# Optimization experiments

Hardware: AMD Instinct MI355X
Metric: run time of the kernel (lower is better)

Reference implementation:

```python
import jax, jax.numpy as jnp
import numpy as np

D_MODEL = 256
NUM_HEADS = 8
D_HEAD = D_MODEL // NUM_HEADS  # 32


def setup_inputs() -> dict:
    key = jax.random.key(0)
    ks = jax.random.split(key, 7)
    N, WH = 8, 2048
    s = 1.0 / np.sqrt(D_MODEL)
    return {
        "x": jax.random.normal(ks[0], (N, WH, D_MODEL), dtype=jnp.float32),
        "Wq": jax.random.normal(ks[1], (D_MODEL, D_MODEL), dtype=jnp.float32) * s,
        "bq": jnp.zeros((D_MODEL,), dtype=jnp.float32),
        "Wk": jax.random.normal(ks[2], (D_MODEL, D_MODEL), dtype=jnp.float32) * s,
        "bk": jnp.zeros((D_MODEL,), dtype=jnp.float32),
        "Wv": jax.random.normal(ks[3], (D_MODEL, D_MODEL), dtype=jnp.float32) * s,
        "bv": jnp.zeros((D_MODEL,), dtype=jnp.float32),
    }


def _mhsa(x, Wq, bq, Wk, bk, Wv, bv):
    N, WH, C = x.shape
    # QKV projections; reshape to (N, heads, WH, d_head)
    def split_heads(t):
        return t.reshape(N, WH, NUM_HEADS, D_HEAD).transpose(0, 2, 1, 3)
    Q = split_heads(x @ Wq + bq)
    K = split_heads(x @ Wk + bk)
    V = split_heads(x @ Wv + bv)
    # FAITHFUL to source: logits /= d_k**(-0.5)  ==  logits * sqrt(d_k)
    logits = jnp.einsum("nhqd,nhkd->nhqk", Q, K) * jnp.sqrt(jnp.float32(D_HEAD))
    attn = jax.nn.softmax(logits, axis=-1)  # dropout p=0.1 is identity in eval
    x_attn = jnp.einsum("nhqk,nhkd->nhqd", attn, V)
    x_attn = x_attn.transpose(0, 2, 1, 3).reshape(N, WH, C)
    # drop_path is identity in eval mode; residual add
    return x_attn + x


def reference(x, Wq, bq, Wk, bk, Wv, bv):
    return _mhsa(x, Wq, bq, Wk, bk, Wv, bv)
```

## Files before the change

### kernel.cpp

```cpp
#include <hip/hip_runtime.h>
#include <math.h>

#define WH 2048
#define DM 256
#define NHD 8
#define DH 32
#define NB 8

typedef __attribute__((ext_vector_type(8))) short short8;
typedef __attribute__((ext_vector_type(4))) short short4v;
typedef __attribute__((ext_vector_type(4))) float f32x4;

__device__ __forceinline__ unsigned short bf16_rn(float f) {
    unsigned u = __float_as_uint(f);
    return (unsigned short)((u + 0x8000u) >> 16);
}
__device__ __forceinline__ float bf16_to_f(unsigned short h) {
    return __uint_as_float(((unsigned)h) << 16);
}
__device__ __forceinline__ unsigned pack_bf16_rn(float f1, float f0) {
    return __builtin_amdgcn_perm(__float_as_uint(f1) + 0x8000u,
                                 __float_as_uint(f0) + 0x8000u, 0x07060302);
}
__device__ __forceinline__ void glds16(const void* g, void* l) {
    __builtin_amdgcn_global_load_lds(
        (const __attribute__((address_space(1))) unsigned int*)g,
        (__attribute__((address_space(3))) unsigned int*)l, 16, 0, 0);
}

__global__ __launch_bounds__(256) void xprep(
    const float* __restrict__ X,
    unsigned short* __restrict__ Xhi, unsigned short* __restrict__ Xlo)
{
    const size_t i = ((size_t)blockIdx.x * 256 + threadIdx.x) * 8;
    float4 a = *(const float4*)&X[i];
    float4 b = *(const float4*)&X[i + 4];
    float v[8] = {a.x, a.y, a.z, a.w, b.x, b.y, b.z, b.w};
    short8 hi, lo;
    #pragma unroll
    for (int e = 0; e < 8; e++) {
        unsigned short hb = bf16_rn(v[e]);
        hi[e] = (short)hb;
        lo[e] = (short)bf16_rn(v[e] - bf16_to_f(hb));
    }
    *(short8*)&Xhi[i] = hi;
    *(short8*)&Xlo[i] = lo;
}

__global__ __launch_bounds__(256) void wprep(
    const float* __restrict__ Wq, const float* __restrict__ Wk,
    const float* __restrict__ Wv,
    unsigned short* __restrict__ WThi, unsigned short* __restrict__ WTlo)
{
    const int z = blockIdx.y;
    const float* W = (z == 0) ? Wq : ((z == 1) ? Wk : Wv);
    const size_t zoff = (size_t)z * DM * DM;
    const int tg = blockIdx.x * 256 + threadIdx.x;
    #pragma unroll
    for (int j = 0; j < 4; j++) {
        const int f = tg + j * 4096;
        const int k  = f >> 6;
        const int n0 = (f & 63) * 4;
        float4 v = *(const float4*)&W[(size_t)k * DM + n0];
        float vv[4] = {v.x, v.y, v.z, v.w};
        #pragma unroll
        for (int i = 0; i < 4; i++) {
            unsigned short hb = bf16_rn(vv[i]);
            WThi[zoff + (size_t)(n0 + i) * DM + k] = hb;
            WTlo[zoff + (size_t)(n0 + i) * DM + k] = bf16_rn(vv[i] - bf16_to_f(hb));
        }
    }
}

#define ASTR 40
__global__ __launch_bounds__(256) void qkv_mfma(
    const unsigned short* __restrict__ Xhi, const unsigned short* __restrict__ Xlo,
    const unsigned short* __restrict__ WThi, const unsigned short* __restrict__ WTlo,
    const float* __restrict__ bq, const float* __restrict__ bk, const float* __restrict__ bv,
    unsigned short* __restrict__ Qhi, unsigned short* __restrict__ Qlo,
    unsigned short* __restrict__ Khi, unsigned short* __restrict__ Klo,
    unsigned short* __restrict__ Vt)
{
    __shared__ __align__(16) char arena[40960];
    unsigned short* Ah = (unsigned short*)arena;
    unsigned short* Al = Ah + 128 * ASTR;
    unsigned short* Bh = Al + 128 * ASTR;
    unsigned short* Bl = Bh + 128 * ASTR;

    const int z = blockIdx.z;
    const float* bias = (z == 0) ? bq : ((z == 1) ? bk : bv);
    const size_t zoff = (size_t)z * DM * DM;

    const int tid  = threadIdx.x;
    const int w    = tid >> 6;
    const int lane = tid & 63;
    const int col  = lane & 15;
    const int quad = lane >> 4;
    const int wr = w >> 1, wc = w & 1;
    const int bm = blockIdx.x * 128;
    const int bn = blockIdx.y * 128;

    f32x4 acc[4][4];
    #pragma unroll
    for (int mi = 0; mi < 4; mi++)
        #pragma unroll
        for (int ni = 0; ni < 4; ni++) acc[mi][ni] = (f32x4){0.f, 0.f, 0.f, 0.f};

    for (int kb = 0; kb < 8; kb++) {
        const int k0 = kb * 32;
        #pragma unroll
        for (int i = 0; i < 2; i++) {
            const int idx = tid + 256 * i;
            const int r  = idx >> 2;
            const int c8 = (idx & 3) * 8;
            *(uint4*)&Ah[r * ASTR + c8] = *(const uint4*)&Xhi[(size_t)(bm + r) * DM + k0 + c8];
            *(uint4*)&Al[r * ASTR + c8] = *(const uint4*)&Xlo[(size_t)(bm + r) * DM + k0 + c8];
            *(uint4*)&Bh[r * ASTR + c8] = *(const uint4*)&WThi[zoff + (size_t)(bn + r) * DM + k0 + c8];
            *(uint4*)&Bl[r * ASTR + c8] = *(const uint4*)&WTlo[zoff + (size_t)(bn + r) * DM + k0 + c8];
        }
        __syncthreads();

        short8 ah[4], al[4], bh[4], bl[4];
        #pragma unroll
        for (int mi = 0; mi < 4; mi++) {
            const int row = wr * 64 + mi * 16 + col;
            ah[mi] = *(const short8*)&Ah[row * ASTR + quad * 8];
            al[mi] = *(const short8*)&Al[row * ASTR + quad * 8];
        }
        #pragma unroll
        for (int ni = 0; ni < 4; ni++) {
            const int nn = wc * 64 + ni * 16 + col;
            bh[ni] = *(const short8*)&Bh[nn * ASTR + quad * 8];
            bl[ni] = *(const short8*)&Bl[nn * ASTR + quad * 8];
        }
        #pragma unroll
        for (int mi = 0; mi < 4; mi++)
            #pragma unroll
            for (int ni = 0; ni < 4; ni++) {
                acc[mi][ni] = __builtin_amdgcn_mfma_f32_16x16x32_bf16(al[mi], bh[ni], acc[mi][ni], 0, 0, 0);
                acc[mi][ni] = __builtin_amdgcn_mfma_f32_16x16x32_bf16(ah[mi], bl[ni], acc[mi][ni], 0, 0, 0);
                acc[mi][ni] = __builtin_amdgcn_mfma_f32_16x16x32_bf16(ah[mi], bh[ni], acc[mi][ni], 0, 0, 0);
            }
        __syncthreads();
    }

    unsigned* Tp = (unsigned*)arena;
    const int n   = bm >> 11;
    const int wqb = bm & (WH - 1);
    const float qsc = (z == 0) ? 8.1611159f : 1.0f;

    #pragma unroll
    for (int p = 0; p < 2; p++) {
        if (wr == p) {
            #pragma unroll
            for (int mi = 0; mi < 4; mi++)
                #pragma unroll
                for (int ni = 0; ni < 4; ni++) {
                    const int lc = wc * 64 + ni * 16 + col;
                    const float bb = bias[bn + lc];
                    #pragma unroll
                    for (int r = 0; r < 4; r++) {
                        float v = (acc[mi][ni][r] + bb) * qsc;
                        unsigned short hb = bf16_rn(v);
                        unsigned short lb = bf16_rn(v - bf16_to_f(hb));
                        Tp[(mi * 16 + quad * 4 + r) * 132 + lc] =
                            (unsigned)hb | ((unsigned)lb << 16);
                    }
                }
        }
        __syncthreads();
        if (z == 2) {
            const int c = tid >> 1, half = tid & 1;
            const int coln = bn + c, h = coln >> 5, d = coln & 31;
            const int tI = (wqb + p * 64 + half * 32) >> 5;
            unsigned short* dst =
                &Vt[(((size_t)(n * NHD + h) * 64 + tI) * 32 + d) * 32];
            unsigned hi[16];
            #pragma unroll
            for (int jj = 0; jj < 16; jj++) {
                unsigned u0 = Tp[(half * 32 + 2 * jj    ) * 132 + c];
                unsigned u1 = Tp[(half * 32 + 2 * jj + 1) * 132 + c];
                hi[jj] = __builtin_amdgcn_perm(u1, u0, 0x05040100);
            }
            #pragma unroll
            for (int s = 0; s < 4; s++)
                *(uint4*)&dst[s * 8] = make_uint4(hi[4*s], hi[4*s+1], hi[4*s+2], hi[4*s+3]);
        } else {
            const int lr = tid >> 2, seg = tid & 3;
            const int coln0 = bn + seg * 32, h = coln0 >> 5;
            const size_t off = ((size_t)((n * NHD + h) * WH) + wqb + p * 64 + lr) * DH;
            unsigned short* Thi = (z == 0) ? Qhi : Khi;
            unsigned short* Tlo = (z == 0) ? Qlo : Klo;
            #pragma unroll
            for (int s = 0; s < 4; s++) {
                unsigned u[8], hi[4], lo[4];
                *(uint4*)&u[0] = *(uint4*)&Tp[lr * 132 + seg * 32 + s * 8];
                *(uint4*)&u[4] = *(uint4*)&Tp[lr * 132 + seg * 32 + s * 8 + 4];
                #pragma unroll
                for (int jj = 0; jj < 4; jj++) {
                    hi[jj] = __builtin_amdgcn_perm(u[2*jj+1], u[2*jj], 0x05040100);
                    lo[jj] = __builtin_amdgcn_perm(u[2*jj+1], u[2*jj], 0x07060302);
                }
                *(uint4*)&Thi[off + s * 8] = make_uint4(hi[0], hi[1], hi[2], hi[3]);
                *(uint4*)&Tlo[off + s * 8] = make_uint4(lo[0], lo[1], lo[2], lo[3]);
            }
        }
        __syncthreads();
    }
}

__global__ __launch_bounds__(256, 4) void attn(
    const unsigned short* __restrict__ Qhi, const unsigned short* __restrict__ Qlo,
    const unsigned short* __restrict__ Khi, const unsigned short* __restrict__ Klo,
    const unsigned short* __restrict__ Vt,  const float* __restrict__ X,
    float* __restrict__ Out)
{
    __shared__ __align__(16) unsigned short Kh[2][1024];
    __shared__ __align__(16) unsigned short Kl[2][1024];
    __shared__ __align__(16) unsigned short Vv[2][1024];

    const int tid  = threadIdx.x;
    const int w    = tid >> 6;
    const int lane = tid & 63;
    const int col  = lane & 15;
    const int quad = lane >> 4;
    const int nh   = blockIdx.y;
    const int q0   = blockIdx.x * 128;
    const size_t base = (size_t)nh * WH * DH;

    short8 qh[2], ql[2];
    #pragma unroll
    for (int f = 0; f < 2; f++) {
        const int qrow = q0 + f * 64 + w * 16 + col;
        qh[f] = *(const short8*)&Qhi[base + (size_t)qrow * DH + quad * 8];
        ql[f] = *(const short8*)&Qlo[base + (size_t)qrow * DH + quad * 8];
    }

    f32x4 ot00 = {0.f,0.f,0.f,0.f}, ot01 = {0.f,0.f,0.f,0.f};
    f32x4 ot10 = {0.f,0.f,0.f,0.f}, ot11 = {0.f,0.f,0.f,0.f};
    float mr0 = -INFINITY, mr1 = -INFINITY, lr0 = 0.f, lr1 = 0.f;

    const char* gb;
    unsigned short *ld0, *ld1;
    if (w == 0)      { gb = (const char*)(Khi + base);        ld0 = &Kh[0][0];   ld1 = &Kh[1][0];   }
    else if (w == 1) { gb = (const char*)(Klo + base);        ld0 = &Kl[0][0];   ld1 = &Kl[1][0];   }
    else if (w == 2) { gb = (const char*)(Vt  + base);        ld0 = &Vv[0][0];   ld1 = &Vv[1][0];   }
    else             { gb = (const char*)(Vt  + base) + 1024; ld0 = &Vv[0][512]; ld1 = &Vv[1][512]; }
    gb += (size_t)lane * 16;

    auto issue = [&](int t, unsigned short* ld) {
        const char* g = gb + (size_t)t * 2048;
        glds16(g, ld);
        if (w < 2) glds16(g + 1024, ld + 512);
    };

    auto body = [&](int b) {
        const short8 kh0 = *(const short8*)&Kh[b][(col     ) * 32 + quad * 8];
        const short8 kh1 = *(const short8*)&Kh[b][(col + 16) * 32 + quad * 8];
        const short8 kl0 = *(const short8*)&Kl[b][(col     ) * 32 + quad * 8];
        const short8 kl1 = *(const short8*)&Kl[b][(col + 16) * 32 + quad * 8];
        const short4v va00 = *(const short4v*)&Vv[b][(col     ) * 32 + quad * 4];
        const short4v va01 = *(const short4v*)&Vv[b][(col     ) * 32 + 16 + quad * 4];
        const short4v va10 = *(const short4v*)&Vv[b][(col + 16) * 32 + quad * 4];
        const short4v va11 = *(const short4v*)&Vv[b][(col + 16) * 32 + 16 + quad * 4];

        #pragma unroll
        for (int f = 0; f < 2; f++) {
            f32x4 s0 = {0.f,0.f,0.f,0.f}, s1 = {0.f,0.f,0.f,0.f};
            s0 = __builtin_amdgcn_mfma_f32_16x16x32_bf16(kh0, ql[f], s0, 0, 0, 0);
            s0 = __builtin_amdgcn_mfma_f32_16x16x32_bf16(kl0, qh[f], s0, 0, 0, 0);
            s0 = __builtin_amdgcn_mfma_f32_16x16x32_bf16(kh0, qh[f], s0, 0, 0, 0);
            s1 = __builtin_amdgcn_mfma_f32_16x16x32_bf16(kh1, ql[f], s1, 0, 0, 0);
            s1 = __builtin_amdgcn_mfma_f32_16x16x32_bf16(kl1, qh[f], s1, 0, 0, 0);
            s1 = __builtin_amdgcn_mfma_f32_16x16x32_bf16(kh1, qh[f], s1, 0, 0, 0);

            float mx = fmaxf(fmaxf(fmaxf(s0[0], s0[1]), fmaxf(s0[2], s0[3])),
                             fmaxf(fmaxf(s1[0], s1[1]), fmaxf(s1[2], s1[3])));
            mx = fmaxf(mx, __shfl_xor(mx, 16));
            mx = fmaxf(mx, __shfl_xor(mx, 32));
            float& mrf = f ? mr1 : mr0;
            float& lrf = f ? lr1 : lr0;
            const float mnew  = fmaxf(mrf, mx);
            const float alpha = __builtin_amdgcn_exp2f(mrf - mnew);

            float p0[4], p1[4], ps = 0.f;
            #pragma unroll
            for (int r = 0; r < 4; r++) {
                p0[r] = __builtin_amdgcn_exp2f(s0[r] - mnew); ps += p0[r];
                p1[r] = __builtin_amdgcn_exp2f(s1[r] - mnew); ps += p1[r];
            }
            ps += __shfl_xor(ps, 16);
            ps += __shfl_xor(ps, 32);
            lrf = lrf * alpha + ps;
            mrf = mnew;

            union { short4v v; unsigned u[2]; } Pb0, Pb1;
            Pb0.u[0] = pack_bf16_rn(p0[1], p0[0]);
            Pb0.u[1] = pack_bf16_rn(p0[3], p0[2]);
            Pb1.u[0] = pack_bf16_rn(p1[1], p1[0]);
            Pb1.u[1] = pack_bf16_rn(p1[3], p1[2]);

            f32x4& o0 = f ? ot10 : ot00;
            f32x4& o1 = f ? ot11 : ot01;
            #pragma unroll
            for (int r = 0; r < 4; r++) { o0[r] *= alpha; o1[r] *= alpha; }
            o0 = __builtin_amdgcn_mfma_f32_16x16x16bf16_1k(va00, Pb0.v, o0, 0, 0, 0);
            o0 = __builtin_amdgcn_mfma_f32_16x16x16bf16_1k(va01, Pb1.v, o0, 0, 0, 0);
            o1 = __builtin_amdgcn_mfma_f32_16x16x16bf16_1k(va10, Pb0.v, o1, 0, 0, 0);
            o1 = __builtin_amdgcn_mfma_f32_16x16x16bf16_1k(va11, Pb1.v, o1, 0, 0, 0);
        }
    };

    issue(0, ld0);
    __syncthreads();
    for (int kt2 = 0; kt2 < 32; kt2++) {
        issue(2 * kt2 + 1, ld1);
        body(0);
        __syncthreads();
        if (kt2 < 31) issue(2 * kt2 + 2, ld0);
        body(1);
        __syncthreads();
    }

    const int n = nh >> 3, h = nh & 7;
    #pragma unroll
    for (int f = 0; f < 2; f++) {
        const float inv = 1.f / (f ? lr1 : lr0);
        const f32x4& o0 = f ? ot10 : ot00;
        const f32x4& o1 = f ? ot11 : ot01;
        const int qrow = q0 + f * 64 + w * 16 + col;
        const size_t a0 = ((size_t)n * WH + qrow) * DM + h * DH + quad * 4;
        float4 x0 = *(const float4*)&X[a0];
        float4 y0;
        y0.x = o0[0] * inv + x0.x;
        y0.y = o0[1] * inv + x0.y;
        y0.z = o0[2] * inv + x0.z;
        y0.w = o0[3] * inv + x0.w;
        *(float4*)&Out[a0] = y0;
        float4 x1 = *(const float4*)&X[a0 + 16];
        float4 y1;
        y1.x = o1[0] * inv + x1.x;
        y1.y = o1[1] * inv + x1.y;
        y1.z = o1[2] * inv + x1.z;
        y1.w = o1[3] * inv + x1.w;
        *(float4*)&Out[a0 + 16] = y1;
    }
}

extern "C" void kernel_launch(void* const* d_in, const int* in_sizes, int n_in,
                              void* d_out, int out_size, void* d_ws, size_t ws_size,
                              hipStream_t stream) {
    const float* x  = (const float*)d_in[0];
    const float* Wq = (const float*)d_in[1];
    const float* bq = (const float*)d_in[2];
    const float* Wk = (const float*)d_in[3];
    const float* bk = (const float*)d_in[4];
    const float* Wv = (const float*)d_in[5];
    const float* bv = (const float*)d_in[6];
    float* out = (float*)d_out;

    const size_t elems = (size_t)NB * WH * DM;
    unsigned short* Qhi  = (unsigned short*)d_ws;
    unsigned short* Qlo  = Qhi + elems;
    unsigned short* Khi  = Qlo + elems;
    unsigned short* Klo  = Khi + elems;
    unsigned short* Vt   = Klo + elems;
    unsigned short* WThi = Vt  + elems;
    unsigned short* WTlo = WThi + (size_t)3 * DM * DM;

    unsigned short* Xhi = (unsigned short*)d_out;
    unsigned short* Xlo = Xhi + elems;

    xprep<<<2048, 256, 0, stream>>>(x, Xhi, Xlo);

    dim3 gw(16, 3);
    wprep<<<gw, 256, 0, stream>>>(Wq, Wk, Wv, WThi, WTlo);

    dim3 gg(128, 2, 3);
    qkv_mfma<<<gg, 256, 0, stream>>>(Xhi, Xlo, WThi, WTlo, bq, bk, bv,
                                     Qhi, Qlo, Khi, Klo, Vt);

    dim3 ga(WH / 128, NB * NHD);
    attn<<<ga, 256, 0, stream>>>(Qhi, Qlo, Khi, Klo, Vt, x, out);
}
```

Baseline: 247.9 us.

## Double-buffer QKV GEMM with async global-to-LDS loads and XOR-swizzled LDS layout

The QKV projection kernel previously staged tiles through registers into padded LDS and synchronized every k-step. It now issues direct global-to-LDS loads into a double buffer, with one wavefront per operand, so the next k-block is prefetched while the current one is computed. The LDS layout becomes unpadded with an XOR swizzle to avoid bank conflicts, and the same swizzle is applied to the K/V tile loads and reads in the attention kernel. The kernel also gets launch_bounds(256,1). The trade-off is a larger LDS footprint (64KB), which lowers occupancy, and the synchronization after each prefetch must stay correct.

```diff
diff --git a/kernel.cpp b/kernel.cpp
--- a/kernel.cpp
+++ b/kernel.cpp
@@ -72,8 +72,7 @@
     }
 }
 
-#define ASTR 40
-__global__ __launch_bounds__(256) void qkv_mfma(
+__global__ __launch_bounds__(256, 1) void qkv_mfma(
     const unsigned short* __restrict__ Xhi, const unsigned short* __restrict__ Xlo,
     const unsigned short* __restrict__ WThi, const unsigned short* __restrict__ WTlo,
     const float* __restrict__ bq, const float* __restrict__ bk, const float* __restrict__ bv,
@@ -81,11 +80,7 @@
     unsigned short* __restrict__ Khi, unsigned short* __restrict__ Klo,
     unsigned short* __restrict__ Vt)
 {
-    __shared__ __align__(16) char arena[40960];
-    unsigned short* Ah = (unsigned short*)arena;
-    unsigned short* Al = Ah + 128 * ASTR;
-    unsigned short* Bh = Al + 128 * ASTR;
-    unsigned short* Bl = Bh + 128 * ASTR;
+    __shared__ __align__(16) unsigned short arena[4 * 2 * 4096];
 
     const int z = blockIdx.z;
     const float* bias = (z == 0) ? bq : ((z == 1) ? bk : bv);
@@ -100,38 +95,48 @@
     const int bm = blockIdx.x * 128;
     const int bn = blockIdx.y * 128;
 
+    const int perm16 = (((lane & 3) ^ ((lane >> 3) & 3))) * 16;
+    const char* glane;
+    if (w == 0)      glane = (const char*)Xhi + (size_t)(bm + (lane >> 2)) * 512 + perm16;
+    else if (w == 1) glane = (const char*)Xlo + (size_t)(bm + (lane >> 2)) * 512 + perm16;
+    else if (w == 2) glane = (const char*)(WThi + zoff) + (size_t)(bn + (lane >> 2)) * 512 + perm16;
+    else             glane = (const char*)(WTlo + zoff) + (size_t)(bn + (lane >> 2)) * 512 + perm16;
+
+    auto issue = [&](int kb, int b) {
+        const char* g0 = glane + (size_t)kb * 64;
+        unsigned short* l0 = &arena[w * 8192 + b * 4096];
+        #pragma unroll
+        for (int g = 0; g < 8; g++)
+            glds16(g0 + (size_t)g * 8192, l0 + g * 512);
+    };
+
     f32x4 acc[4][4];
     #pragma unroll
     for (int mi = 0; mi < 4; mi++)
         #pragma unroll
         for (int ni = 0; ni < 4; ni++) acc[mi][ni] = (f32x4){0.f, 0.f, 0.f, 0.f};
 
+    const int sw = (col >> 1) & 3;
+    const int fO = (quad ^ sw) * 8;
+
+    issue(0, 0);
+    __syncthreads();
     for (int kb = 0; kb < 8; kb++) {
-        const int k0 = kb * 32;
-        #pragma unroll
-        for (int i = 0; i < 2; i++) {
-            const int idx = tid + 256 * i;
-            const int r  = idx >> 2;
-            const int c8 = (idx & 3) * 8;
-            *(uint4*)&Ah[r * ASTR + c8] = *(const uint4*)&Xhi[(size_t)(bm + r) * DM + k0 + c8];
-            *(uint4*)&Al[r * ASTR + c8] = *(const uint4*)&Xlo[(size_t)(bm + r) * DM + k0 + c8];
-            *(uint4*)&Bh[r * ASTR + c8] = *(const uint4*)&WThi[zoff + (size_t)(bn + r) * DM + k0 + c8];
-            *(uint4*)&Bl[r * ASTR + c8] = *(const uint4*)&WTlo[zoff + (size_t)(bn + r) * DM + k0 + c8];
-        }
-        __syncthreads();
+        const int b = kb & 1;
+        if (kb < 7) issue(kb + 1, b ^ 1);
 
         short8 ah[4], al[4], bh[4], bl[4];
         #pragma unroll
         for (int mi = 0; mi < 4; mi++) {
-            const int row = wr * 64 + mi * 16 + col;
-            ah[mi] = *(const short8*)&Ah[row * ASTR + quad * 8];
-            al[mi] = *(const short8*)&Al[row * ASTR + quad * 8];
+            const int ro = (wr * 64 + mi * 16 + col) * 32 + fO;
+            ah[mi] = *(const short8*)&arena[        b * 4096 + ro];
+            al[mi] = *(const short8*)&arena[ 8192 + b * 4096 + ro];
         }
         #pragma unroll
         for (int ni = 0; ni < 4; ni++) {
-            const int nn = wc * 64 + ni * 16 + col;
-            bh[ni] = *(const short8*)&Bh[nn * ASTR + quad * 8];
-            bl[ni] = *(const short8*)&Bl[nn * ASTR + quad * 8];
+            const int no = (wc * 64 + ni * 16 + col) * 32 + fO;
+            bh[ni] = *(const short8*)&arena[16384 + b * 4096 + no];
+            bl[ni] = *(const short8*)&arena[24576 + b * 4096 + no];
         }
         #pragma unroll
         for (int mi = 0; mi < 4; mi++)
@@ -240,13 +245,14 @@
     f32x4 ot10 = {0.f,0.f,0.f,0.f}, ot11 = {0.f,0.f,0.f,0.f};
     float mr0 = -INFINITY, mr1 = -INFINITY, lr0 = 0.f, lr1 = 0.f;
 
+    const size_t toff = (size_t)(lane >> 2) * 64 + (((lane & 3) ^ ((lane >> 3) & 3))) * 16;
     const char* gb;
     unsigned short *ld0, *ld1;
     if (w == 0)      { gb = (const char*)(Khi + base);        ld0 = &Kh[0][0];   ld1 = &Kh[1][0];   }
     else if (w == 1) { gb = (const char*)(Klo + base);        ld0 = &Kl[0][0];   ld1 = &Kl[1][0];   }
     else if (w == 2) { gb = (const char*)(Vt  + base);        ld0 = &Vv[0][0];   ld1 = &Vv[1][0];   }
     else             { gb = (const char*)(Vt  + base) + 1024; ld0 = &Vv[0][512]; ld1 = &Vv[1][512]; }
-    gb += (size_t)lane * 16;
+    gb += toff;
 
     auto issue = [&](int t, unsigned short* ld) {
         const char* g = gb + (size_t)t * 2048;
@@ -254,15 +260,20 @@
         if (w < 2) glds16(g + 1024, ld + 512);
     };
 
+    const int sw  = (col >> 1) & 3;
+    const int kO0 = col * 32 + (quad ^ sw) * 8;
+    const int vO0 = col * 32 + ((quad >> 1) ^ sw) * 8 + (quad & 1) * 4;
+    const int vO1 = col * 32 + ((2 + (quad >> 1)) ^ sw) * 8 + (quad & 1) * 4;
+
     auto body = [&](int b) {
-        const short8 kh0 = *(const short8*)&Kh[b][(col     ) * 32 + quad * 8];
-        const short8 kh1 = *(const short8*)&Kh[b][(col + 16) * 32 + quad * 8];
-        const short8 kl0 = *(const short8*)&Kl[b][(col     ) * 32 + quad * 8];
-        const short8 kl1 = *(const short8*)&Kl[b][(col + 16) * 32 + quad * 8];
-        const short4v va00 = *(const short4v*)&Vv[b][(col     ) * 32 + quad * 4];
-        const short4v va01 = *(const short4v*)&Vv[b][(col     ) * 32 + 16 + quad * 4];
-        const short4v va10 = *(const short4v*)&Vv[b][(col + 16) * 32 + quad * 4];
-        const short4v va11 = *(const short4v*)&Vv[b][(col + 16) * 32 + 16 + quad * 4];
+        const short8 kh0 = *(const short8*)&Kh[b][kO0];
+        const short8 kh1 = *(const short8*)&Kh[b][kO0 + 512];
+        const short8 kl0 = *(const short8*)&Kl[b][kO0];
+        const short8 kl1 = *(const short8*)&Kl[b][kO0 + 512];
+        const short4v va00 = *(const short4v*)&Vv[b][vO0];
+        const short4v va01 = *(const short4v*)&Vv[b][vO1];
+        const short4v va10 = *(const short4v*)&Vv[b][vO0 + 512];
+        const short4v va11 = *(const short4v*)&Vv[b][vO1 + 512];
 
         #pragma unroll
         for (int f = 0; f < 2; f++) {
```

Result: faster. 232.6 us (-6.2%).
